# Kernel optimization log

Measured on AMD Instinct MI355X. Metric: run time of the kernel, lower is better.

## Reference

```python
import jax, jax.numpy as jnp
import numpy as np

D_MODEL = 1024
N_HEADS = 16
D_HEAD = D_MODEL // N_HEADS
SCALE = D_HEAD ** -0.5


def setup_inputs() -> dict:
    key = jax.random.key(0)
    ks = jax.random.split(key, 9)
    s = 0.02
    x = jax.random.normal(ks[0], (2, 2048, D_MODEL), dtype=jnp.float32)
    Wq = jax.random.normal(ks[1], (D_MODEL, D_MODEL), dtype=jnp.float32) * s
    Wk = jax.random.normal(ks[2], (D_MODEL, D_MODEL), dtype=jnp.float32) * s
    Wv = jax.random.normal(ks[3], (D_MODEL, D_MODEL), dtype=jnp.float32) * s
    Wo = jax.random.normal(ks[4], (D_MODEL, D_MODEL), dtype=jnp.float32) * s
    bq = jax.random.normal(ks[5], (D_MODEL,), dtype=jnp.float32) * s
    bk = jax.random.normal(ks[6], (D_MODEL,), dtype=jnp.float32) * s
    bv = jax.random.normal(ks[7], (D_MODEL,), dtype=jnp.float32) * s
    bo = jax.random.normal(ks[8], (D_MODEL,), dtype=jnp.float32) * s
    return {"x": x, "Wq": Wq, "bq": bq, "Wk": Wk, "bk": bk,
            "Wv": Wv, "bv": bv, "Wo": Wo, "bo": bo}


def reference(x, Wq, bq, Wk, bk, Wv, bv, Wo, bo):
    B, S, _ = x.shape
    # torch nn.Linear: y = x @ W.T + b
    def proj(W, b):
        h = jnp.einsum('bsd,ed->bse', x, W) + b
        return h.reshape(B, S, N_HEADS, D_HEAD).transpose(0, 2, 1, 3)  # [B,H,S,Dh]
    Q = proj(Wq, bq)
    K = proj(Wk, bk)
    V = proj(Wv, bv)
    # chunked QK^T softmax over full K == full attention (no mask, dropout=0)
    scores = jnp.einsum('bhqd,bhkd->bhqk', Q, K) * SCALE  # [B,H,S,S]
    attn = jax.nn.softmax(scores, axis=-1)
    out = jnp.einsum('bhqk,bhkd->bhqd', attn, V)
    out = out.transpose(0, 2, 1, 3).reshape(B, S, D_MODEL)
    return jnp.einsum('bsd,ed->bse', out, Wo) + bo
```

## Files before the change

### kernel.cpp

```cpp
#include <hip/hip_runtime.h>
#include <cstdint>
#include <cstddef>


typedef unsigned short u16;
typedef unsigned int u32;
typedef __bf16 bf16x8 __attribute__((ext_vector_type(8)));
typedef float f32x4 __attribute__((ext_vector_type(4)));

#define GLOAD_LDS16(gp, lp)                                                            \
  __builtin_amdgcn_global_load_lds((const __attribute__((address_space(1))) void*)(gp),\
                                   (__attribute__((address_space(3))) void*)(lp),      \
                                   16, 0, 0)

__device__ __forceinline__ u16 f2bf(float f) {
  unsigned u = __builtin_bit_cast(unsigned, f);
  u = u + 0x7fffu + ((u >> 16) & 1u);
  return (u16)(u >> 16);
}

__device__ __forceinline__ u32 pack_bf2(float a, float b) {
  u32 ua = __builtin_bit_cast(u32, a) + 0x8000u;
  u32 ub = __builtin_bit_cast(u32, b) + 0x8000u;
  return __builtin_amdgcn_perm(ub, ua, 0x07060302u);
}

#define QSCALE 0.1803368801111204f

__global__ void cvt_all(const float* __restrict__ x,
                        const float* __restrict__ wq, const float* __restrict__ wk,
                        const float* __restrict__ wv, const float* __restrict__ wo,
                        u16* __restrict__ xb, u16* __restrict__ wqb,
                        u16* __restrict__ wkb, u16* __restrict__ wvb,
                        u16* __restrict__ wob) {
  int bx = blockIdx.x;
  const float* s; u16* d; int off;
  if (bx < 2048)      { s = x;  d = xb;  off = bx; }
  else if (bx < 2560) { s = wq; d = wqb; off = bx - 2048; }
  else if (bx < 3072) { s = wk; d = wkb; off = bx - 2560; }
  else if (bx < 3584) { s = wv; d = wvb; off = bx - 3072; }
  else                { s = wo; d = wob; off = bx - 3584; }
  int i = off * 2048 + threadIdx.x * 8;
  float4 a = *(const float4*)(s + i);
  float4 b = *(const float4*)(s + i + 4);
  uint4 o;
  o.x = f2bf(a.x) | ((u32)f2bf(a.y) << 16);
  o.y = f2bf(a.z) | ((u32)f2bf(a.w) << 16);
  o.z = f2bf(b.x) | ((u32)f2bf(b.y) << 16);
  o.w = f2bf(b.z) | ((u32)f2bf(b.w) << 16);
  *(uint4*)(d + i) = o;
}

template <int MODE>
__global__ __launch_bounds__(256, 3) void gemm_mfma(
    const u16* __restrict__ A,
    const u16* __restrict__ W0, const u16* __restrict__ W1, const u16* __restrict__ W2,
    const float* __restrict__ b0, const float* __restrict__ b1, const float* __restrict__ b2,
    u16* __restrict__ o0, u16* __restrict__ o1, u16* __restrict__ o2,
    float* __restrict__ oF)
{
  __shared__ __align__(16) u16 As[128 * 64];
  __shared__ __align__(16) u16 Bs[128 * 64];

  const int tid = threadIdx.x;
  const int w = tid >> 6, l = tid & 63;
  const int lane = l & 15, quad = l >> 4;
  const int wm = w >> 1, wn = w & 1;
  const int m0 = blockIdx.y * 128;
  const int n0g = blockIdx.x * 128;

  const int src = (MODE == 0) ? (n0g >> 10) : 0;
  const u16* Wsel = (MODE == 0) ? (src == 0 ? W0 : (src == 1 ? W1 : W2)) : W0;
  const float* bsel = (MODE == 0) ? (src == 0 ? b0 : (src == 1 ? b1 : b2)) : b0;
  const int n_base = (MODE == 0) ? (n0g & 1023) : n0g;

  const int c8 = ((l & 7) ^ (l >> 3)) * 8;

  f32x4 acc[4][4] = {};

  for (int kt = 0; kt < 1024; kt += 64) {
    __syncthreads();
    const u16* Ag = A + (size_t)m0 * 1024 + kt;
    const u16* Bg = Wsel + (size_t)n_base * 1024 + kt;
    #pragma unroll
    for (int i = 0; i < 4; ++i) {
      int rr = w * 32 + i * 8;
      GLOAD_LDS16(Ag + (size_t)(rr + (l >> 3)) * 1024 + c8, As + rr * 64);
      GLOAD_LDS16(Bg + (size_t)(rr + (l >> 3)) * 1024 + c8, Bs + rr * 64);
    }
    __syncthreads();

    bf16x8 af[4][2], bf[4][2];
    #pragma unroll
    for (int mf = 0; mf < 4; ++mf)
      #pragma unroll
      for (int ks = 0; ks < 2; ++ks) {
        af[mf][ks] = *(const bf16x8*)((const char*)As +
            (wm * 64 + mf * 16 + lane) * 128 + (((ks * 4 + quad) ^ (lane & 7)) * 16));
        bf[mf][ks] = *(const bf16x8*)((const char*)Bs +
            (wn * 64 + mf * 16 + lane) * 128 + (((ks * 4 + quad) ^ (lane & 7)) * 16));
      }
    #pragma unroll
    for (int ks = 0; ks < 2; ++ks)
      #pragma unroll
      for (int mf = 0; mf < 4; ++mf)
        #pragma unroll
        for (int nf = 0; nf < 4; ++nf)
          acc[mf][nf] = __builtin_amdgcn_mfma_f32_16x16x32_bf16(
              af[mf][ks], bf[nf][ks], acc[mf][nf], 0, 0, 0);
  }

  float bb[4];
  #pragma unroll
  for (int nf = 0; nf < 4; ++nf) bb[nf] = bsel[n_base + wn * 64 + nf * 16 + lane];

  u16* osel = (MODE == 0) ? (src == 0 ? o0 : (src == 1 ? o1 : o2)) : o0;

  #pragma unroll
  for (int mf = 0; mf < 4; ++mf) {
    int mb = m0 + wm * 64 + mf * 16 + quad * 4;
    #pragma unroll
    for (int nf = 0; nf < 4; ++nf) {
      int n_l = wn * 64 + nf * 16 + lane;
      if (MODE == 0 && src == 2) {
        float v0 = acc[mf][nf][0] + bb[nf];
        float v1 = acc[mf][nf][1] + bb[nf];
        float v2 = acc[mf][nf][2] + bb[nf];
        float v3 = acc[mf][nf][3] + bb[nf];
        int bi = mb >> 11, s = mb & 2047;
        int n_in = n_base + n_l;
        int h = n_in >> 6, dh = n_in & 63;
        uint2 pk = make_uint2(pack_bf2(v0, v1), pack_bf2(v2, v3));
        *(uint2*)(o2 + (((size_t)(bi * 16 + h) * 64 + dh) * 2048 + s)) = pk;
      } else {
        #pragma unroll
        for (int r = 0; r < 4; ++r) {
          float v = acc[mf][nf][r] + bb[nf];
          int m = mb + r;
          if (MODE == 0) {
            if (src == 0) v *= QSCALE;
            int bi = m >> 11, s = m & 2047;
            int n_in = n_base + n_l;
            int h = n_in >> 6, dh = n_in & 63;
            osel[(((size_t)(bi * 16 + h) * 2048 + s) << 6) + dh] = f2bf(v);
          } else {
            oF[(size_t)m * 1024 + n0g + n_l] = v;
          }
        }
      }
    }
  }
}

union SMemU {
  struct {
    u16 K[3][64 * 64];
    u16 V[3][64 * 64];
  } m;
  struct {
    float O[4][32 * 64];
    float L[4][32];
  } f;
};

__global__ __launch_bounds__(512, 4) void attn_mfma(
    const u16* __restrict__ Qg_, const u16* __restrict__ Kg_,
    const u16* __restrict__ VTg_, u16* __restrict__ Og)
{
  __shared__ __align__(16) SMemU sm;

  const int tid = threadIdx.x;
  const int w = tid >> 6, l = tid & 63;
  const int lane = l & 15, quad = l >> 4;
  const int g = w >> 1;
  const int kh = w & 1;
  const int bh = blockIdx.y;
  const int q0 = blockIdx.x * 128;

  const u16* Qg  = Qg_ + ((size_t)bh * 2048 + q0 + g * 32) * 64;
  const u16* Kg  = Kg_ + (size_t)bh * 2048 * 64;
  const u16* VTg = VTg_ + (size_t)bh * 64 * 2048;

  const int c8 = ((l & 7) ^ (l >> 3)) * 8;
  const int lrow = l >> 3;
  const int rr = w * 8;

  bf16x8 bq[2][2];
  #pragma unroll
  for (int qf = 0; qf < 2; ++qf)
    #pragma unroll
    for (int ks = 0; ks < 2; ++ks)
      bq[qf][ks] = *(const bf16x8*)(Qg +
          (size_t)(qf * 16 + lane) * 64 + ks * 32 + quad * 8);

  GLOAD_LDS16(Kg + (size_t)(rr + lrow) * 64 + c8, sm.m.K[0] + rr * 64);
  GLOAD_LDS16(VTg + (size_t)(rr + lrow) * 2048 + c8, sm.m.V[0] + rr * 64);
  GLOAD_LDS16(Kg + (size_t)(64 + rr + lrow) * 64 + c8, sm.m.K[1] + rr * 64);
  GLOAD_LDS16(VTg + (size_t)(rr + lrow) * 2048 + 64 + c8, sm.m.V[1] + rr * 64);

  f32x4 oa[2][4] = {};
  float lsum[2] = {0.f, 0.f};
  int cur = 0;

  for (int kt = 0; kt < 32; ++kt) {
    if (kt < 31) asm volatile("s_waitcnt vmcnt(2)" ::: "memory");
    else         asm volatile("s_waitcnt vmcnt(0)" ::: "memory");
    __builtin_amdgcn_s_barrier();
    asm volatile("" ::: "memory");

    if (kt < 30) {
      int pf = (cur == 0) ? 2 : cur - 1;
      GLOAD_LDS16(Kg + (size_t)((kt + 2) * 64 + rr + lrow) * 64 + c8,
                  sm.m.K[pf] + rr * 64);
      GLOAD_LDS16(VTg + (size_t)(rr + lrow) * 2048 + (kt + 2) * 64 + c8,
                  sm.m.V[pf] + rr * 64);
    }

    f32x4 sa[2][2] = {};
    #pragma unroll
    for (int ks = 0; ks < 2; ++ks) {
      bf16x8 ak[2];
      #pragma unroll
      for (int kf = 0; kf < 2; ++kf)
        ak[kf] = *(const bf16x8*)((const char*)sm.m.K[cur] +
            (kh * 32 + kf * 16 + lane) * 128 + (((ks * 4 + quad) ^ (lane & 7)) * 16));
      #pragma unroll
      for (int kf = 0; kf < 2; ++kf)
        #pragma unroll
        for (int qf = 0; qf < 2; ++qf)
          sa[kf][qf] = __builtin_amdgcn_mfma_f32_16x16x32_bf16(
              ak[kf], bq[qf][ks], sa[kf][qf], 0, 0, 0);
    }

    bf16x8 ap[2];
    #pragma unroll
    for (int qf = 0; qf < 2; ++qf) {
      float x0 = __builtin_amdgcn_exp2f(sa[0][qf][0]);
      float x1 = __builtin_amdgcn_exp2f(sa[0][qf][1]);
      float x2 = __builtin_amdgcn_exp2f(sa[0][qf][2]);
      float x3 = __builtin_amdgcn_exp2f(sa[0][qf][3]);
      float y0 = __builtin_amdgcn_exp2f(sa[1][qf][0]);
      float y1 = __builtin_amdgcn_exp2f(sa[1][qf][1]);
      float y2 = __builtin_amdgcn_exp2f(sa[1][qf][2]);
      float y3 = __builtin_amdgcn_exp2f(sa[1][qf][3]);
      lsum[qf] += ((x0 + x1) + (x2 + x3)) + ((y0 + y1) + (y2 + y3));
      u32 X0 = pack_bf2(x0, x1), X1 = pack_bf2(x2, x3);
      u32 Y0 = pack_bf2(y0, y1), Y1 = pack_bf2(y2, y3);
      asm("v_permlane32_swap_b32 %0, %1" : "+v"(X0), "+v"(Y0));
      asm("v_permlane16_swap_b32 %0, %1" : "+v"(X0), "+v"(Y0));
      asm("v_permlane32_swap_b32 %0, %1" : "+v"(X1), "+v"(Y1));
      asm("v_permlane16_swap_b32 %0, %1" : "+v"(X1), "+v"(Y1));
      uint4 d4 = make_uint4(X0, X1, Y0, Y1);
      ap[qf] = __builtin_bit_cast(bf16x8, d4);
    }

    {
      bf16x8 bv[4];
      #pragma unroll
      for (int df = 0; df < 4; ++df)
        bv[df] = *(const bf16x8*)((const char*)sm.m.V[cur] +
            (df * 16 + lane) * 128 + (((kh * 4 + quad) ^ (lane & 7)) * 16));
      #pragma unroll
      for (int qf = 0; qf < 2; ++qf)
        #pragma unroll
        for (int df = 0; df < 4; ++df)
          oa[qf][df] = __builtin_amdgcn_mfma_f32_16x16x32_bf16(
              ap[qf], bv[df], oa[qf][df], 0, 0, 0);
    }

    cur = (cur == 2) ? 0 : cur + 1;
  }

  #pragma unroll
  for (int qf = 0; qf < 2; ++qf) {
    lsum[qf] += __shfl_xor(lsum[qf], 16);
    lsum[qf] += __shfl_xor(lsum[qf], 32);
  }

  __syncthreads();
  if (kh == 1) {
    #pragma unroll
    for (int qf = 0; qf < 2; ++qf)
      #pragma unroll
      for (int df = 0; df < 4; ++df)
        #pragma unroll
        for (int r = 0; r < 4; ++r)
          sm.f.O[g][(qf * 16 + quad * 4 + r) * 64 + df * 16 + lane] = oa[qf][df][r];
    if (l < 16) {
      sm.f.L[g][l] = lsum[0];
      sm.f.L[g][16 + l] = lsum[1];
    }
  }
  __syncthreads();
  if (kh == 0) {
    const int b = bh >> 4, hh = bh & 15;
    u16* Ob = Og + ((size_t)b * 2048 + q0 + g * 32) * 1024 + hh * 64;
    float ltot[2];
    #pragma unroll
    for (int qf = 0; qf < 2; ++qf)
      ltot[qf] = lsum[qf] + sm.f.L[g][qf * 16 + lane];
    #pragma unroll
    for (int qf = 0; qf < 2; ++qf)
      #pragma unroll
      for (int r = 0; r < 4; ++r) {
        float inv = 1.0f / __shfl(ltot[qf], quad * 4 + r, 16);
        int qrow = qf * 16 + quad * 4 + r;
        #pragma unroll
        for (int df = 0; df < 4; ++df) {
          float v = oa[qf][df][r] + sm.f.O[g][qrow * 64 + df * 16 + lane];
          Ob[(size_t)qrow * 1024 + df * 16 + lane] = f2bf(v * inv);
        }
      }
  }
}

extern "C" void kernel_launch(void* const* d_in, const int* in_sizes, int n_in,
                              void* d_out, int out_size, void* d_ws, size_t ws_size,
                              hipStream_t stream)
{
  (void)in_sizes; (void)n_in; (void)out_size; (void)ws_size;
  const float* x  = (const float*)d_in[0];
  const float* Wq = (const float*)d_in[1];
  const float* bq = (const float*)d_in[2];
  const float* Wk = (const float*)d_in[3];
  const float* bk = (const float*)d_in[4];
  const float* Wv = (const float*)d_in[5];
  const float* bv = (const float*)d_in[6];
  const float* Wo = (const float*)d_in[7];
  const float* bo = (const float*)d_in[8];
  float* y = (float*)d_out;

  const size_t NM = (size_t)4096 * 1024;
  u16* xb  = (u16*)d_ws;
  u16* wqb = xb + NM;
  u16* wkb = wqb + 1024 * 1024;
  u16* wvb = wkb + 1024 * 1024;
  u16* wob = wvb + 1024 * 1024;
  u16* Qb  = wob + 1024 * 1024;
  u16* Kb  = Qb + NM;
  u16* VTb = Kb + NM;
  u16* AOb = VTb + NM;

  cvt_all<<<4096, 256, 0, stream>>>(x, Wq, Wk, Wv, Wo, xb, wqb, wkb, wvb, wob);

  gemm_mfma<0><<<dim3(24, 32), 256, 0, stream>>>(
      xb, wqb, wkb, wvb, bq, bk, bv, Qb, Kb, VTb, nullptr);

  attn_mfma<<<dim3(16, 32), 512, 0, stream>>>(Qb, Kb, VTb, AOb);

  gemm_mfma<1><<<dim3(8, 32), 256, 0, stream>>>(
      AOb, wob, nullptr, nullptr, bo, nullptr, nullptr,
      nullptr, nullptr, nullptr, y);
}
```

Measured before the change: 182.1 us.

## Store Q transposed with packed stores and halve M tile for output GEMM

The QKV projection epilogue now writes Q in a transposed [B,H,Dh,S] layout using packed 4-element stores, as it already did for V, replacing scattered 2-byte stores. The attention kernel gathers its Q fragments from that transposed layout with strided scalar loads. The GEMM is templated on BM, and the output projection uses BM=64 to double the number of blocks (8x64 grid), which should fill more CUs. The costs are uncoalesced Q loads in attention and lower per-block reuse in the output GEMM.

```diff
diff --git a/kernel.cpp b/kernel.cpp
--- a/kernel.cpp
+++ b/kernel.cpp
@@ -51,7 +51,7 @@
   *(uint4*)(d + i) = o;
 }
 
-template <int MODE>
+template <int MODE, int BM>
 __global__ __launch_bounds__(256, 3) void gemm_mfma(
     const u16* __restrict__ A,
     const u16* __restrict__ W0, const u16* __restrict__ W1, const u16* __restrict__ W2,
@@ -59,14 +59,17 @@
     u16* __restrict__ o0, u16* __restrict__ o1, u16* __restrict__ o2,
     float* __restrict__ oF)
 {
-  __shared__ __align__(16) u16 As[128 * 64];
+  constexpr int MF = BM / 32;
+  constexpr int AG = BM / 32;
+
+  __shared__ __align__(16) u16 As[BM * 64];
   __shared__ __align__(16) u16 Bs[128 * 64];
 
   const int tid = threadIdx.x;
   const int w = tid >> 6, l = tid & 63;
   const int lane = l & 15, quad = l >> 4;
   const int wm = w >> 1, wn = w & 1;
-  const int m0 = blockIdx.y * 128;
+  const int m0 = blockIdx.y * BM;
   const int n0g = blockIdx.x * 128;
 
   const int src = (MODE == 0) ? (n0g >> 10) : 0;
@@ -75,35 +78,43 @@
   const int n_base = (MODE == 0) ? (n0g & 1023) : n0g;
 
   const int c8 = ((l & 7) ^ (l >> 3)) * 8;
-
-  f32x4 acc[4][4] = {};
+  const int lrow = l >> 3;
+
+  f32x4 acc[MF][4] = {};
 
   for (int kt = 0; kt < 1024; kt += 64) {
     __syncthreads();
     const u16* Ag = A + (size_t)m0 * 1024 + kt;
     const u16* Bg = Wsel + (size_t)n_base * 1024 + kt;
     #pragma unroll
+    for (int i = 0; i < AG; ++i) {
+      int rr = w * (8 * AG) + i * 8;
+      GLOAD_LDS16(Ag + (size_t)(rr + lrow) * 1024 + c8, As + rr * 64);
+    }
+    #pragma unroll
     for (int i = 0; i < 4; ++i) {
       int rr = w * 32 + i * 8;
-      GLOAD_LDS16(Ag + (size_t)(rr + (l >> 3)) * 1024 + c8, As + rr * 64);
-      GLOAD_LDS16(Bg + (size_t)(rr + (l >> 3)) * 1024 + c8, Bs + rr * 64);
+      GLOAD_LDS16(Bg + (size_t)(rr + lrow) * 1024 + c8, Bs + rr * 64);
     }
     __syncthreads();
 
-    bf16x8 af[4][2], bf[4][2];
-    #pragma unroll
-    for (int mf = 0; mf < 4; ++mf)
-      #pragma unroll
-      for (int ks = 0; ks < 2; ++ks) {
+    bf16x8 af[MF][2], bf[4][2];
+    #pragma unroll
+    for (int mf = 0; mf < MF; ++mf)
+      #pragma unroll
+      for (int ks = 0; ks < 2; ++ks)
         af[mf][ks] = *(const bf16x8*)((const char*)As +
-            (wm * 64 + mf * 16 + lane) * 128 + (((ks * 4 + quad) ^ (lane & 7)) * 16));
-        bf[mf][ks] = *(const bf16x8*)((const char*)Bs +
-            (wn * 64 + mf * 16 + lane) * 128 + (((ks * 4 + quad) ^ (lane & 7)) * 16));
-      }
+            (wm * (BM / 2) + mf * 16 + lane) * 128 + (((ks * 4 + quad) ^ (lane & 7)) * 16));
+    #pragma unroll
+    for (int nf = 0; nf < 4; ++nf)
+      #pragma unroll
+      for (int ks = 0; ks < 2; ++ks)
+        bf[nf][ks] = *(const bf16x8*)((const char*)Bs +
+            (wn * 64 + nf * 16 + lane) * 128 + (((ks * 4 + quad) ^ (lane & 7)) * 16));
     #pragma unroll
     for (int ks = 0; ks < 2; ++ks)
       #pragma unroll
-      for (int mf = 0; mf < 4; ++mf)
+      for (int mf = 0; mf < MF; ++mf)
         #pragma unroll
         for (int nf = 0; nf < 4; ++nf)
           acc[mf][nf] = __builtin_amdgcn_mfma_f32_16x16x32_bf16(
@@ -117,28 +128,28 @@
   u16* osel = (MODE == 0) ? (src == 0 ? o0 : (src == 1 ? o1 : o2)) : o0;
 
   #pragma unroll
-  for (int mf = 0; mf < 4; ++mf) {
-    int mb = m0 + wm * 64 + mf * 16 + quad * 4;
+  for (int mf = 0; mf < MF; ++mf) {
+    int mb = m0 + wm * (BM / 2) + mf * 16 + quad * 4;
     #pragma unroll
     for (int nf = 0; nf < 4; ++nf) {
       int n_l = wn * 64 + nf * 16 + lane;
-      if (MODE == 0 && src == 2) {
-        float v0 = acc[mf][nf][0] + bb[nf];
-        float v1 = acc[mf][nf][1] + bb[nf];
-        float v2 = acc[mf][nf][2] + bb[nf];
-        float v3 = acc[mf][nf][3] + bb[nf];
+      if (MODE == 0 && src != 1) {
+        float sc = (src == 0) ? QSCALE : 1.0f;
+        float v0 = (acc[mf][nf][0] + bb[nf]) * sc;
+        float v1 = (acc[mf][nf][1] + bb[nf]) * sc;
+        float v2 = (acc[mf][nf][2] + bb[nf]) * sc;
+        float v3 = (acc[mf][nf][3] + bb[nf]) * sc;
         int bi = mb >> 11, s = mb & 2047;
         int n_in = n_base + n_l;
         int h = n_in >> 6, dh = n_in & 63;
         uint2 pk = make_uint2(pack_bf2(v0, v1), pack_bf2(v2, v3));
-        *(uint2*)(o2 + (((size_t)(bi * 16 + h) * 64 + dh) * 2048 + s)) = pk;
+        *(uint2*)(osel + (((size_t)(bi * 16 + h) * 64 + dh) * 2048 + s)) = pk;
       } else {
         #pragma unroll
         for (int r = 0; r < 4; ++r) {
           float v = acc[mf][nf][r] + bb[nf];
           int m = mb + r;
           if (MODE == 0) {
-            if (src == 0) v *= QSCALE;
             int bi = m >> 11, s = m & 2047;
             int n_in = n_base + n_l;
             int h = n_in >> 6, dh = n_in & 63;
@@ -177,7 +188,7 @@
   const int bh = blockIdx.y;
   const int q0 = blockIdx.x * 128;
 
-  const u16* Qg  = Qg_ + ((size_t)bh * 2048 + q0 + g * 32) * 64;
+  const u16* QTg = Qg_ + (size_t)bh * 64 * 2048;
   const u16* Kg  = Kg_ + (size_t)bh * 2048 * 64;
   const u16* VTg = VTg_ + (size_t)bh * 64 * 2048;
 
@@ -185,13 +196,19 @@
   const int lrow = l >> 3;
   const int rr = w * 8;
 
+  const int qcol = q0 + g * 32 + lane;
   bf16x8 bq[2][2];
   #pragma unroll
   for (int qf = 0; qf < 2; ++qf)
     #pragma unroll
-    for (int ks = 0; ks < 2; ++ks)
-      bq[qf][ks] = *(const bf16x8*)(Qg +
-          (size_t)(qf * 16 + lane) * 64 + ks * 32 + quad * 8);
+    for (int ks = 0; ks < 2; ++ks) {
+      bf16x8 v;
+      #pragma unroll
+      for (int j = 0; j < 8; ++j)
+        v[j] = __builtin_bit_cast(__bf16,
+            QTg[(size_t)(ks * 32 + quad * 8 + j) * 2048 + qcol + qf * 16]);
+      bq[qf][ks] = v;
+    }
 
   GLOAD_LDS16(Kg + (size_t)(rr + lrow) * 64 + c8, sm.m.K[0] + rr * 64);
   GLOAD_LDS16(VTg + (size_t)(rr + lrow) * 2048 + c8, sm.m.V[0] + rr * 64);
@@ -343,12 +360,12 @@
 
   cvt_all<<<4096, 256, 0, stream>>>(x, Wq, Wk, Wv, Wo, xb, wqb, wkb, wvb, wob);
 
-  gemm_mfma<0><<<dim3(24, 32), 256, 0, stream>>>(
+  gemm_mfma<0, 128><<<dim3(24, 32), 256, 0, stream>>>(
       xb, wqb, wkb, wvb, bq, bk, bv, Qb, Kb, VTb, nullptr);
 
   attn_mfma<<<dim3(16, 32), 512, 0, stream>>>(Qb, Kb, VTb, AOb);
 
-  gemm_mfma<1><<<dim3(8, 32), 256, 0, stream>>>(
+  gemm_mfma<1, 64><<<dim3(8, 64), 256, 0, stream>>>(
       AOb, wob, nullptr, nullptr, bo, nullptr, nullptr,
       nullptr, nullptr, nullptr, y);
 }
```

Result: no change. 184.1 us (+1.1%).
